# Kernel tuning notes

Measured on AMD Instinct MI355X. Metric: run time of the kernel, lower is better.

The kernel has to match this reference:

```python
import jax, jax.numpy as jnp
import numpy as np

WORKSPACE_RADIUS = 1.0
WORKSPACE_HEIGHT = 1.0


def setup_inputs() -> dict:
    key = jax.random.key(0)
    k1, k2 = jax.random.split(key)
    # (B, N, 6): xyz + normals, already padded to common length N
    pointclouds = jax.random.normal(k1, (32, 131072, 6), dtype=jnp.float32)
    # (B, 4, 4): homogeneous task transforms
    task_transform = jax.random.normal(k2, (32, 4, 4), dtype=jnp.float32)
    return {"pointclouds": pointclouds, "task_transform": task_transform}


def reference(pointclouds, task_transform):
    # Split xyz points and normals
    pts = pointclouds[..., :3]          # (B, N, 3)
    nrm = pointclouds[..., 3:]          # (B, N, 3)

    rot = task_transform[:, :3, :3]     # (B, 3, 3)
    trans = task_transform[:, :3, 3]    # (B, 3)

    # points @ rotation + translation (matches torch.matmul(points, rotation))
    p = jnp.einsum('bnd,bde->bne', pts, rot) + trans[:, None, :]

    # padded rows have all-zero normals
    non_padded = jnp.sum(nrm, axis=-1) != 0

    sq_dist = p[..., 0] ** 2 + p[..., 1] ** 2
    in_range = (sq_dist < WORKSPACE_RADIUS ** 2) & (p[..., 2] < WORKSPACE_HEIGHT)
    valid = in_range & non_padded      # (B, N)

    # Filter-and-repad: compact valid points to the front (stable = order
    # preserving, as in the torch boolean-index version), zero the tail.
    order = jnp.argsort(~valid, axis=1, stable=True)                 # (B, N)
    gathered = jnp.take_along_axis(pointclouds, order[..., None], axis=1)
    mask_sorted = jnp.take_along_axis(valid, order, axis=1)
    return gathered * mask_sorted[..., None].astype(pointclouds.dtype)
```

## Files before the change

### kernel.cpp

```cpp
#include <hip/hip_runtime.h>
#include <cstdint>

namespace {

constexpr int kB   = 32;
constexpr int kN   = 131072;
constexpr int kC   = 6;
constexpr int TPB  = 256;
constexpr int ROWS_PER_BLK = 512;
constexpr int BPB  = kN / ROWS_PER_BLK;
constexpr int NBLK = kB * BPB;
constexpr int WAVES = TPB / 64;

__device__ __forceinline__ int waveSum(int v) {
#pragma unroll
    for (int off = 32; off; off >>= 1) v += __shfl_xor(v, off, 64);
    return v;
}

__global__ __launch_bounds__(TPB) void k_count(const float* __restrict__ pc,
                                               const float* __restrict__ tt,
                                               uint64_t* __restrict__ masks,
                                               int* __restrict__ blkCnt) {
    const int blk  = blockIdx.x;
    const int b    = blk >> 8;
    const int tid  = threadIdx.x;
    const int lane = tid & 63;
    const int wv   = tid >> 6;

    const float* T = tt + b * 16;
    const float T0 = T[0], T1 = T[1], T2 = T[2],  T3  = T[3];
    const float T4 = T[4], T5 = T[5], T6 = T[6],  T7  = T[7];
    const float T8 = T[8], T9 = T[9], T10 = T[10], T11 = T[11];

    const float4* f4 = (const float4*)pc + (size_t)blk * (ROWS_PER_BLK * kC / 4);
    const float4 q0 = f4[3 * tid];
    const float4 q1 = f4[3 * tid + 1];
    const float4 q2 = f4[3 * tid + 2];

    const float ns0 = (q0.w + q1.x) + q1.y;
    const float px0 = q0.x * T0 + q0.y * T4 + q0.z * T8  + T3;
    const float py0 = q0.x * T1 + q0.y * T5 + q0.z * T9  + T7;
    const float pz0 = q0.x * T2 + q0.y * T6 + q0.z * T10 + T11;
    const bool v0 = (px0 * px0 + py0 * py0 < 1.0f) && (pz0 < 1.0f) && (ns0 != 0.0f);

    const float ns1 = (q2.y + q2.z) + q2.w;
    const float px1 = q1.z * T0 + q1.w * T4 + q2.x * T8  + T3;
    const float py1 = q1.z * T1 + q1.w * T5 + q2.x * T9  + T7;
    const float pz1 = q1.z * T2 + q1.w * T6 + q2.x * T10 + T11;
    const bool v1 = (px1 * px1 + py1 * py1 < 1.0f) && (pz1 < 1.0f) && (ns1 != 0.0f);

    const uint64_t m0 = __ballot(v0);
    const uint64_t m1 = __ballot(v1);

    __shared__ uint64_t sm[WAVES * 2];
    if (lane == 0) {
        sm[wv * 2]     = m0;
        sm[wv * 2 + 1] = m1;
        masks[(size_t)blk * 8 + wv * 2]     = m0;
        masks[(size_t)blk * 8 + wv * 2 + 1] = m1;
    }
    __syncthreads();
    if (wv == 0) {
        int v = (lane < 8) ? __popcll(sm[lane]) : 0;
        v = waveSum(v);
        if (lane == 0) blkCnt[blk] = v;
    }
}

__global__ __launch_bounds__(TPB) void k_scatter(const float* __restrict__ pc,
                                                 const uint64_t* __restrict__ masks,
                                                 const int* __restrict__ blkCnt,
                                                 float* __restrict__ out) {
    const int blk  = blockIdx.x;
    const int b    = blk >> 8;
    const int sub  = blk & (BPB - 1);
    const int tid  = threadIdx.x;
    const int lane = tid & 63;
    const int wv   = tid >> 6;

    __shared__ uint64_t sm[8];
    __shared__ int sRed[2 * WAVES];

    if (tid < 8) sm[tid] = masks[(size_t)blk * 8 + tid];

    const int c = blkCnt[b * BPB + tid];
    const int pw = waveSum((tid < sub) ? c : 0);
    const int tw = waveSum(c);
    if (lane == 0) { sRed[wv] = pw; sRed[WAVES + wv] = tw; }
    __syncthreads();
    const int blockBase = (sRed[0] + sRed[1]) + (sRed[2] + sRed[3]);
    const int total     = (sRed[4] + sRed[5]) + (sRed[6] + sRed[7]);

    const uint64_t m0 = sm[wv * 2], m1 = sm[wv * 2 + 1];
    int wb = 0;
#pragma unroll
    for (int w = 0; w < WAVES - 1; ++w)
        if (w < wv) wb += __popcll(sm[w * 2]) + __popcll(sm[w * 2 + 1]);

    const uint64_t low = (1ull << lane) - 1ull;
    const int beforeE = __popcll(m0 & low) + __popcll(m1 & low);
    const bool v0 = (m0 >> lane) & 1ull;
    const bool v1 = (m1 >> lane) & 1ull;

    const size_t batchF = (size_t)b * kN * kC;
    const int rowBlk = sub * ROWS_PER_BLK + wv * 128 + 2 * lane;
    const int vcnt0 = blockBase + wb + beforeE;
    const int vcnt1 = vcnt0 + (v0 ? 1 : 0);

    if (v0) {
        const float2* r = (const float2*)(pc + batchF + (size_t)rowBlk * kC);
        float2* o = (float2*)(out + batchF + (size_t)vcnt0 * kC);
        o[0] = r[0]; o[1] = r[1]; o[2] = r[2];
    }
    if (v1) {
        const float2* r = (const float2*)(pc + batchF + (size_t)(rowBlk + 1) * kC);
        float2* o = (float2*)(out + batchF + (size_t)vcnt1 * kC);
        o[0] = r[0]; o[1] = r[1]; o[2] = r[2];
    }

    const int tail = kN - total;
    const int len  = (tail + BPB - 1) >> 8;
    const int r0 = total + sub * len;
    const int r1 = min(r0 + len, kN);
    if (r0 < r1) {
        float2* o2 = (float2*)(out + batchF);
        const float2 zz = make_float2(0.0f, 0.0f);
        const int e0 = r0 * 3, e1 = r1 * 3;
        for (int i = e0 + tid; i < e1; i += TPB) o2[i] = zz;
    }
}

}

extern "C" void kernel_launch(void* const* d_in, const int* in_sizes, int n_in,
                              void* d_out, int out_size, void* d_ws, size_t ws_size,
                              hipStream_t stream) {
    const float* pc = (const float*)d_in[0];
    const float* tt = (const float*)d_in[1];
    float* out = (float*)d_out;

    uint64_t* masks = (uint64_t*)d_ws;
    int* blkCnt     = (int*)((char*)d_ws + (size_t)NBLK * 8 * sizeof(uint64_t));

    k_count<<<NBLK, TPB, 0, stream>>>(pc, tt, masks, blkCnt);
    k_scatter<<<NBLK, TPB, 0, stream>>>(pc, masks, blkCnt, out);
}
```

Before: 39.41 us.

## Switch scatter to output-driven gather with coalesced LDS-staged loads and stores

The count kernel now loads its tile with fully coalesced float4 reads into shared memory and then reads per-thread rows from LDS. The emit kernel is inverted from input-scatter to output-gather: each thread owns two output rows, binary-searches a block prefix array and then the mask bits to find the source row, and the whole output tile is written through LDS with coalesced float4 stores. This also writes the zero tail in the same pass. The cost is a two-level search per output row, plus dependent, uncoalesced source reads for valid rows.

```diff
diff --git a/kernel.cpp b/kernel.cpp
--- a/kernel.cpp
+++ b/kernel.cpp
@@ -11,6 +11,7 @@
 constexpr int BPB  = kN / ROWS_PER_BLK;
 constexpr int NBLK = kB * BPB;
 constexpr int WAVES = TPB / 64;
+constexpr int F4_PER_BLK = ROWS_PER_BLK * kC / 4;
 
 __device__ __forceinline__ int waveSum(int v) {
 #pragma unroll
@@ -33,10 +34,18 @@
     const float T4 = T[4], T5 = T[5], T6 = T[6],  T7  = T[7];
     const float T8 = T[8], T9 = T[9], T10 = T[10], T11 = T[11];
 
-    const float4* f4 = (const float4*)pc + (size_t)blk * (ROWS_PER_BLK * kC / 4);
-    const float4 q0 = f4[3 * tid];
-    const float4 q1 = f4[3 * tid + 1];
-    const float4 q2 = f4[3 * tid + 2];
+    const float4* f4 = (const float4*)pc + (size_t)blk * F4_PER_BLK;
+    const float4 qa = f4[tid];
+    const float4 qb = f4[tid + 256];
+    const float4 qc = f4[tid + 512];
+
+    __shared__ float4 sb[F4_PER_BLK];
+    sb[tid] = qa; sb[tid + 256] = qb; sb[tid + 512] = qc;
+    __syncthreads();
+
+    const float4 q0 = sb[3 * tid];
+    const float4 q1 = sb[3 * tid + 1];
+    const float4 q2 = sb[3 * tid + 2];
 
     const float ns0 = (q0.w + q1.x) + q1.y;
     const float px0 = q0.x * T0 + q0.y * T4 + q0.z * T8  + T3;
@@ -68,10 +77,10 @@
     }
 }
 
-__global__ __launch_bounds__(TPB) void k_scatter(const float* __restrict__ pc,
-                                                 const uint64_t* __restrict__ masks,
-                                                 const int* __restrict__ blkCnt,
-                                                 float* __restrict__ out) {
+__global__ __launch_bounds__(TPB) void k_emit(const float* __restrict__ pc,
+                                              const uint64_t* __restrict__ masks,
+                                              const int* __restrict__ blkCnt,
+                                              float* __restrict__ out) {
     const int blk  = blockIdx.x;
     const int b    = blk >> 8;
     const int sub  = blk & (BPB - 1);
@@ -79,56 +88,84 @@
     const int lane = tid & 63;
     const int wv   = tid >> 6;
 
-    __shared__ uint64_t sm[8];
-    __shared__ int sRed[2 * WAVES];
-
-    if (tid < 8) sm[tid] = masks[(size_t)blk * 8 + tid];
+    __shared__ int pre[BPB];
+    __shared__ int wsum[WAVES];
+    __shared__ int s_tot;
+    __shared__ float4 xb[F4_PER_BLK];
 
     const int c = blkCnt[b * BPB + tid];
-    const int pw = waveSum((tid < sub) ? c : 0);
-    const int tw = waveSum(c);
-    if (lane == 0) { sRed[wv] = pw; sRed[WAVES + wv] = tw; }
+    int v = c;
+#pragma unroll
+    for (int off = 1; off < 64; off <<= 1) {
+        const int u = __shfl_up(v, off, 64);
+        if (lane >= off) v += u;
+    }
+    if (lane == 63) wsum[wv] = v;
     __syncthreads();
-    const int blockBase = (sRed[0] + sRed[1]) + (sRed[2] + sRed[3]);
-    const int total     = (sRed[4] + sRed[5]) + (sRed[6] + sRed[7]);
-
-    const uint64_t m0 = sm[wv * 2], m1 = sm[wv * 2 + 1];
-    int wb = 0;
+    int wbase = 0;
 #pragma unroll
     for (int w = 0; w < WAVES - 1; ++w)
-        if (w < wv) wb += __popcll(sm[w * 2]) + __popcll(sm[w * 2 + 1]);
+        if (w < wv) wbase += wsum[w];
+    pre[tid] = wbase + v - c;
+    if (tid == TPB - 1) s_tot = wbase + v;
+    __syncthreads();
+    const int total = s_tot;
 
-    const uint64_t low = (1ull << lane) - 1ull;
-    const int beforeE = __popcll(m0 & low) + __popcll(m1 & low);
-    const bool v0 = (m0 >> lane) & 1ull;
-    const bool v1 = (m1 >> lane) & 1ull;
-
-    const size_t batchF = (size_t)b * kN * kC;
-    const int rowBlk = sub * ROWS_PER_BLK + wv * 128 + 2 * lane;
-    const int vcnt0 = blockBase + wb + beforeE;
-    const int vcnt1 = vcnt0 + (v0 ? 1 : 0);
-
-    if (v0) {
-        const float2* r = (const float2*)(pc + batchF + (size_t)rowBlk * kC);
-        float2* o = (float2*)(out + batchF + (size_t)vcnt0 * kC);
-        o[0] = r[0]; o[1] = r[1]; o[2] = r[2];
-    }
-    if (v1) {
-        const float2* r = (const float2*)(pc + batchF + (size_t)(rowBlk + 1) * kC);
-        float2* o = (float2*)(out + batchF + (size_t)vcnt1 * kC);
-        o[0] = r[0]; o[1] = r[1]; o[2] = r[2];
+    const int r0 = sub * ROWS_PER_BLK + 2 * tid;
+    float2 val[6];
+#pragma unroll
+    for (int e = 0; e < 2; ++e) {
+        const int r = r0 + e;
+        float2 x0 = make_float2(0.0f, 0.0f), x1 = x0, x2 = x0;
+        if (r < total) {
+            int lo = 0, hi = BPB - 1;
+#pragma unroll
+            for (int it = 0; it < 8; ++it) {
+                const int mid = (lo + hi + 1) >> 1;
+                if (pre[mid] <= r) lo = mid; else hi = mid - 1;
+            }
+            int local = r - pre[lo];
+            const uint64_t* M = masks + (size_t)(b * BPB + lo) * 8;
+            int w2 = 0;
+#pragma unroll
+            for (int w = 0; w < 3; ++w) {
+                const int cnt = __popcll(M[2 * w]) + __popcll(M[2 * w + 1]);
+                if (local >= cnt && w2 == w) { local -= cnt; w2 = w + 1; }
+            }
+            const uint64_t m0 = M[2 * w2], m1 = M[2 * w2 + 1];
+            int L = 0;
+#pragma unroll
+            for (int s = 32; s; s >>= 1) {
+                const int t2 = L + s;
+                if (t2 <= 63) {
+                    const uint64_t below = (1ull << t2) - 1ull;
+                    const int g = __popcll(m0 & below) + __popcll(m1 & below);
+                    if (g <= local) L = t2;
+                }
+            }
+            const uint64_t belowL = (1ull << L) - 1ull;
+            const int gL = __popcll(m0 & belowL) + __popcll(m1 & belowL);
+            const int rem = local - gL;
+            const int b0 = (int)((m0 >> L) & 1ull);
+            const int e2 = (rem == 1 || !b0) ? 1 : 0;
+            const int row = lo * ROWS_PER_BLK + w2 * 128 + 2 * L + e2;
+            const float2* s2 = (const float2*)pc + ((size_t)b * kN + (size_t)row) * 3;
+            x0 = s2[0]; x1 = s2[1]; x2 = s2[2];
+        }
+        val[3 * e]     = x0;
+        val[3 * e + 1] = x1;
+        val[3 * e + 2] = x2;
     }
 
-    const int tail = kN - total;
-    const int len  = (tail + BPB - 1) >> 8;
-    const int r0 = total + sub * len;
-    const int r1 = min(r0 + len, kN);
-    if (r0 < r1) {
-        float2* o2 = (float2*)(out + batchF);
-        const float2 zz = make_float2(0.0f, 0.0f);
-        const int e0 = r0 * 3, e1 = r1 * 3;
-        for (int i = e0 + tid; i < e1; i += TPB) o2[i] = zz;
-    }
+    float2* x2l = (float2*)xb;
+#pragma unroll
+    for (int k = 0; k < 6; ++k) x2l[6 * tid + k] = val[k];
+    __syncthreads();
+
+    float4* o4 = (float4*)(out + ((size_t)b * kN + (size_t)sub * ROWS_PER_BLK) * kC);
+    o4[tid]       = xb[tid];
+    o4[tid + 256] = xb[tid + 256];
+    o4[tid + 512] = xb[tid + 512];
 }
 
 }
@@ -144,5 +181,5 @@
     int* blkCnt     = (int*)((char*)d_ws + (size_t)NBLK * 8 * sizeof(uint64_t));
 
     k_count<<<NBLK, TPB, 0, stream>>>(pc, tt, masks, blkCnt);
-    k_scatter<<<NBLK, TPB, 0, stream>>>(pc, masks, blkCnt, out);
+    k_emit<<<NBLK, TPB, 0, stream>>>(pc, masks, blkCnt, out);
 }
```

After: 40.48 us. +2.7%, slower.
